# Kernel optimization log

Hardware: AMD Instinct MI355X
Metric: run time of the kernel (lower is better)

The kernel has to match this reference:

```python
import jax, jax.numpy as jnp
import numpy as np

PAD_token, SOS_token, EOS_token = 0, 1, 2
V, E, H, B, To, Ti = 10000, 512, 512, 32, 256, 1024


def _u(key, shape, fan_in):
    s = 1.0 / np.sqrt(fan_in)
    return jax.random.uniform(key, shape, jnp.float32, -s, s)


def setup_inputs() -> dict:
    key = jax.random.key(0)
    ks = jax.random.split(key, 16)
    inp = {
        "padded_input": jax.random.randint(ks[0], (B, To), 3, V),
        "encoder_padded_outputs": jax.random.normal(ks[1], (B, Ti, H), jnp.float32),
        "embedding": jax.random.normal(ks[2], (V, E), jnp.float32) * 0.02,
        # layer 0 LSTMCell: input = embed + encoder context (E + H)
        "Wih0": _u(ks[3], (4 * H, E + H), H), "Whh0": _u(ks[4], (4 * H, H), H),
        "bih0": _u(ks[5], (4 * H,), H),       "bhh0": _u(ks[6], (4 * H,), H),
        # layer 1 LSTMCell: input = H
        "Wih1": _u(ks[7], (4 * H, H), H),     "Whh1": _u(ks[8], (4 * H, H), H),
        "bih1": _u(ks[9], (4 * H,), H),       "bhh1": _u(ks[10], (4 * H,), H),
        # MLP: Linear(2H -> H), Tanh, Linear(H -> V)
        "W1": _u(ks[11], (H, 2 * H), 2 * H),  "b1": _u(ks[12], (H,), 2 * H),
        "W2": _u(ks[13], (V, H), H),          "b2": _u(ks[14], (V,), H),
    }
    return inp


def _lstm_cell(x, h, c, Wih, Whh, bih, bhh):
    g = x @ Wih.T + bih + h @ Whh.T + bhh            # [B, 4H]
    i, f, gg, o = jnp.split(g, 4, axis=-1)           # torch gate order i,f,g,o
    c2 = jax.nn.sigmoid(f) * c + jax.nn.sigmoid(i) * jnp.tanh(gg)
    h2 = jax.nn.sigmoid(o) * jnp.tanh(c2)
    return h2, c2


def reference(padded_input, encoder_padded_outputs, embedding,
              Wih0, Whh0, bih0, bhh0, Wih1, Whh1, bih1, bhh1,
              W1, b1, W2, b2):
    n = padded_input.shape[0]
    sos = jnp.full((n, 1), SOS_token, padded_input.dtype)
    eos = jnp.full((n, 1), EOS_token, padded_input.dtype)
    ys_in = jnp.concatenate([sos, padded_input], axis=1)   # [B, To+1]
    ys_out = jnp.concatenate([padded_input, eos], axis=1)  # [B, To+1]

    emb = embedding[ys_in]                                 # [B, To+1, E]
    emb_t = jnp.swapaxes(emb, 0, 1)                        # [To+1, B, E]
    enc = encoder_padded_outputs                           # [B, Ti, H]

    h0 = jnp.zeros((n, H), enc.dtype)
    init = (h0, h0, h0, h0, jnp.zeros((n, enc.shape[2]), enc.dtype))

    def step(carry, e_t):
        h_0, c_0, h_1, c_1, att_c = carry
        rnn_in = jnp.concatenate([e_t, att_c], axis=1)
        h_0, c_0 = _lstm_cell(rnn_in, h_0, c_0, Wih0, Whh0, bih0, bhh0)
        h_1, c_1 = _lstm_cell(h_0, h_1, c_1, Wih1, Whh1, bih1, bhh1)
        scores = jnp.einsum('bh,bth->bt', h_1, enc)        # [B, Ti]
        att_w = jax.nn.softmax(scores, axis=-1)
        att_c = jnp.einsum('bt,bth->bh', att_w, enc)       # [B, H]
        mlp_in = jnp.concatenate([h_1, att_c], axis=1)
        logits = jnp.tanh(mlp_in @ W1.T + b1) @ W2.T + b2  # [B, V]
        return (h_0, c_0, h_1, c_1, att_c), logits

    _, y_all = jax.lax.scan(step, init, emb_t)             # [To+1, B, V]
    logits = jnp.swapaxes(y_all, 0, 1).reshape(-1, V)      # [B*(To+1), V]
    labels = ys_out.reshape(-1)
    logp = jax.nn.log_softmax(logits, axis=-1)
    nll = -jnp.take_along_axis(logp, labels[:, None], axis=1)[:, 0]
    mask = (labels != PAD_token).astype(logits.dtype)
    loss = jnp.sum(nll * mask) / jnp.maximum(jnp.sum(mask), 1.0)
    return loss
```

## Files before the change

kernel.cpp:

```cpp
#include <hip/hip_runtime.h>
#include <hip/hip_bf16.h>

#define B_    32
#define TO_   256
#define T_    257
#define H_    512
#define V_    10000
#define TI_   1024
#define NROW_ 8224
#define NB_   256

using f32x4 = __attribute__((ext_vector_type(4))) float;
using s16x8 = __attribute__((ext_vector_type(8))) short;
typedef unsigned long long ull;

struct Ptrs {
  const int* padded;
  const float* enc;
  const float* emb;
  const float *Wih0, *Whh0, *bih0, *bhh0;
  const float *Wih1, *Whh1, *bih1, *bhh1;
  const float *W1, *b1, *W2, *b2;
  float* out;
  unsigned short *mlpin;
  unsigned short *embt;
  unsigned short *tanhv;
  unsigned short *W0c;
  unsigned short *W1c;
  unsigned short *W1b;
  unsigned short *W2b;
  float *bias0c, *bias1c;
  unsigned short *attc;
  float *upart;
  float *zp;
  unsigned short *Xh0;
  unsigned short *Xh1;
  float *Xh1f;
  unsigned *arrX;
  unsigned *arrY;
  unsigned *marr;
  unsigned *larr;
  unsigned *ibar;
  float *rowsum;
  float *lablog;
};

__device__ __forceinline__ unsigned short f2b(float f){
  __hip_bfloat16 h = __float2bfloat16(f);
  unsigned short r; __builtin_memcpy(&r, &h, 2); return r;
}
__device__ __forceinline__ float b2f(unsigned short u){
  unsigned v = ((unsigned)u) << 16; float f; __builtin_memcpy(&f, &v, 4); return f;
}
__device__ __forceinline__ float sigf(float x){ return 1.f / (1.f + expf(-x)); }

__device__ __forceinline__ float aldf(const float* p){
  return __hip_atomic_load(p, __ATOMIC_RELAXED, __HIP_MEMORY_SCOPE_AGENT);
}
__device__ __forceinline__ unsigned aldw(const unsigned* p){
  return __hip_atomic_load(p, __ATOMIC_RELAXED, __HIP_MEMORY_SCOPE_AGENT);
}
__device__ __forceinline__ ull aldu(const ull* p){
  return __hip_atomic_load(p, __ATOMIC_RELAXED, __HIP_MEMORY_SCOPE_AGENT);
}
__device__ __forceinline__ void astf(float* p, float v){
  __hip_atomic_store(p, v, __ATOMIC_RELAXED, __HIP_MEMORY_SCOPE_AGENT);
}
__device__ __forceinline__ void astu(ull* p, ull v){
  __hip_atomic_store(p, v, __ATOMIC_RELAXED, __HIP_MEMORY_SCOPE_AGENT);
}
__device__ __forceinline__ void astw(unsigned* p, unsigned v){
  __hip_atomic_store(p, v, __ATOMIC_RELAXED, __HIP_MEMORY_SCOPE_AGENT);
}
#define DRAIN asm volatile("s_waitcnt vmcnt(0)" ::: "memory")

__device__ __forceinline__ void gbarInit(unsigned* bar){
  DRAIN; __syncthreads();
  if (threadIdx.x < 64){
    const int l = threadIdx.x;
    if (l == 0) astw(bar + blockIdx.x * 4, 1u);
    for (;;){
      unsigned f0 = aldw(bar + (l      ) * 4);
      unsigned f1 = aldw(bar + (l +  64) * 4);
      unsigned f2 = aldw(bar + (l + 128) * 4);
      unsigned f3 = aldw(bar + (l + 192) * 4);
      if (__all((f0 >= 1u) & (f1 >= 1u) & (f2 >= 1u) & (f3 >= 1u))) break;
      __builtin_amdgcn_s_sleep(1);
    }
  }
  __syncthreads();
}

__global__ __launch_bounds__(256) void kprep(Ptrs P){
  const int stride = gridDim.x * blockDim.x;
  const int i0 = blockIdx.x * blockDim.x + threadIdx.x;
  for (int i = i0; i < 128 * 4; i += stride){ P.arrX[i] = 0u; P.arrY[i] = 0u; }
  for (int i = i0; i < 256 * 4; i += stride){ P.marr[i] = 0u; P.ibar[i] = 0u; }
  for (int i = i0; i < 32 * 4; i += stride) P.larr[i] = 0u;
  for (int i = i0; i < T_ * B_ * 512; i += stride){
    int k = i & 511, tb = i >> 9, b = tb & 31, t = tb >> 5;
    int tok = (t == 0) ? 1 : P.padded[b * TO_ + (t - 1)];
    P.embt[i] = f2b(P.emb[(size_t)tok * 512 + k]);
  }
  for (int i = i0; i < 2048 * 1536; i += stride){
    int k = i % 1536, gp = i / 1536;
    int j = gp >> 2, q = gp & 3, g = q * 512 + j;
    float v = (k < 1024) ? P.Wih0[(size_t)g * 1024 + k] : P.Whh0[(size_t)g * 512 + (k - 1024)];
    P.W0c[i] = f2b(v);
  }
  for (int i = i0; i < 2048 * 1024; i += stride){
    int k = i & 1023, gp = i >> 10;
    int j = gp >> 2, q = gp & 3, g = q * 512 + j;
    float v = (k < 512) ? P.Wih1[(size_t)g * 512 + k] : P.Whh1[(size_t)g * 512 + (k - 512)];
    P.W1c[i] = f2b(v);
  }
  for (int i = i0; i < 2048; i += stride){
    int j = i >> 2, q = i & 3, g = q * 512 + j;
    P.bias0c[i] = P.bih0[g] + P.bhh0[g];
    P.bias1c[i] = P.bih1[g] + P.bhh1[g];
  }
  for (int i = i0; i < 512 * 1024; i += stride) P.W1b[i] = f2b(P.W1[i]);
  for (int i = i0; i < NROW_; i += stride) P.rowsum[i] = 0.f;
}

__global__ __launch_bounds__(256) void kprep2(Ptrs P){
  const int stride = gridDim.x * blockDim.x;
  const int i0 = blockIdx.x * blockDim.x + threadIdx.x;
  for (int i = i0; i < V_ * 512; i += stride) P.W2b[i] = f2b(P.W2[i]);
}

__global__ __launch_bounds__(256, 1) void kA(Ptrs P){
  __shared__ __align__(16) unsigned short enc_s[128 * 512];
  __shared__ float h1_s[512];
  __shared__ float w_s[128];
  __shared__ float gate_s[2][32][17];
  __shared__ float h_s[32][4];
  __shared__ float zred[2];
  const int bb = blockIdx.x, tid = threadIdx.x;
  const int b_att = bb >> 3, tc = bb & 7;

  {
    const float* ep = P.enc + ((size_t)b_att * TI_ + (size_t)tc * 128) * H_;
    for (int idx = tid; idx < 128 * 512; idx += 256){
      int r = idx >> 9;
      unsigned byteoff = ((unsigned)idx * 2u) ^ ((unsigned)(r & 7) << 4);
      enc_s[byteoff >> 1] = f2b(ep[idx]);
    }
  }
  {
    int g = bb * 256 + tid;
    if (g < 16384){ astw((unsigned*)P.Xh0 + g, 0u); astw((unsigned*)P.Xh1 + g, 0u); }
    if (g < 32768) astf(P.Xh1f + g, 0.f);
    if (g < 8192)  astw((unsigned*)P.attc + g, 0u);
  }
  gbarInit(P.ibar);

  const int wv = tid >> 6, l = tid & 63, lr = l & 15, lk = l >> 4;
  const int bh = wv & 1, kh = wv >> 1;
  const int batch = bh * 16 + lr;
  const int eidx = tid - 128, eb = eidx >> 2, ejl = eidx & 3;
  const bool isGemm = bb < 128;
  const int rb = bb - 128; const bool isRed = (rb >= 0 && rb < 32);
  float c0r = 0.f, c1r = 0.f;

  for (int t = 0; t < T_; ++t){
    const int p = t & 1, pp = p ^ 1;
    const unsigned tv = (unsigned)t + 1u;
    if (isGemm){
      if (t > 0 && tid < 64){
        const unsigned want = tv - 1u;
        for (;;){
          unsigned f = (tid < 32) ? aldw(P.larr + tid * 4) : want;
          if (__all(f >= want)) break;
          __builtin_amdgcn_s_sleep(1);
        }
      }
      __syncthreads();
      {
        const unsigned short* Brow = P.W0c + (size_t)(bb * 16 + lr) * 1536;
        const unsigned short* Erow = P.embt + ((size_t)t * 32 + batch) * 512;
        const ull* Arow = (const ull*)(P.attc + batch * 512);
        const ull* Hrow = (const ull*)(P.Xh0 + pp * 16384 + batch * 512);
        f32x4 acc = {0.f, 0.f, 0.f, 0.f};
        #pragma unroll
        for (int ks = 0; ks < 8; ++ks){
          const int kb = (kh * 8 + ks) * 32 + lk * 8;
          s16x8 a = *(const s16x8*)(Erow + kb);
          s16x8 b = *(const s16x8*)(Brow + kb);
          acc = __builtin_amdgcn_mfma_f32_16x16x32_bf16(a, b, acc, 0, 0, 0);
        }
        #pragma unroll
        for (int ks = 0; ks < 8; ++ks){
          const int kb = (kh * 8 + ks) * 32 + lk * 8;
          ull d0 = aldu(Arow + (kb >> 2)), d1 = aldu(Arow + (kb >> 2) + 1);
          s16x8 a; __builtin_memcpy(&a, &d0, 8); __builtin_memcpy(((char*)&a) + 8, &d1, 8);
          s16x8 b = *(const s16x8*)(Brow + 512 + kb);
          acc = __builtin_amdgcn_mfma_f32_16x16x32_bf16(a, b, acc, 0, 0, 0);
        }
        #pragma unroll
        for (int ks = 0; ks < 8; ++ks){
          const int kb = (kh * 8 + ks) * 32 + lk * 8;
          ull d0 = aldu(Hrow + (kb >> 2)), d1 = aldu(Hrow + (kb >> 2) + 1);
          s16x8 a; __builtin_memcpy(&a, &d0, 8); __builtin_memcpy(((char*)&a) + 8, &d1, 8);
          s16x8 b = *(const s16x8*)(Brow + 1024 + kb);
          acc = __builtin_amdgcn_mfma_f32_16x16x32_bf16(a, b, acc, 0, 0, 0);
        }
        #pragma unroll
        for (int j = 0; j < 4; ++j) gate_s[kh][bh * 16 + lk * 4 + j][lr] = acc[j];
      }
      __syncthreads();
      if (tid >= 128){
        const float* bs = P.bias0c + bb * 16 + ejl * 4;
        float ii = sigf (gate_s[0][eb][ejl * 4 + 0] + gate_s[1][eb][ejl * 4 + 0] + bs[0]);
        float ff = sigf (gate_s[0][eb][ejl * 4 + 1] + gate_s[1][eb][ejl * 4 + 1] + bs[1]);
        float gg = tanhf(gate_s[0][eb][ejl * 4 + 2] + gate_s[1][eb][ejl * 4 + 2] + bs[2]);
        float oo = sigf (gate_s[0][eb][ejl * 4 + 3] + gate_s[1][eb][ejl * 4 + 3] + bs[3]);
        float cn = ff * c0r + ii * gg; c0r = cn;
        h_s[eb][ejl] = oo * tanhf(cn);
      }
      __syncthreads();
      if (tid < 32){
        unsigned short hb[4];
        #pragma unroll
        for (int jl = 0; jl < 4; ++jl) hb[jl] = f2b(h_s[tid][jl]);
        ull v; __builtin_memcpy(&v, hb, 8);
        astu((ull*)(P.Xh0 + p * 16384 + tid * 512 + bb * 4), v);
      }
      DRAIN; __syncthreads();
      if (tid < 64){
        if (tid == 0) astw(P.arrX + bb * 4, tv);
        for (;;){
          unsigned f0 = aldw(P.arrX + tid * 4), f1 = aldw(P.arrX + (tid + 64) * 4);
          if (__all((f0 >= tv) & (f1 >= tv))) break;
          __builtin_amdgcn_s_sleep(1);
        }
      }
      __syncthreads();
      {
        const unsigned short* Brow = P.W1c + (size_t)(bb * 16 + lr) * 1024;
        const ull* H0r = (const ull*)(P.Xh0 + p * 16384 + batch * 512);
        const ull* H1r = (const ull*)(P.Xh1 + pp * 16384 + batch * 512);
        f32x4 acc = {0.f, 0.f, 0.f, 0.f};
        #pragma unroll
        for (int ks = 0; ks < 8; ++ks){
          const int kb = (kh * 8 + ks) * 32 + lk * 8;
          ull d0 = aldu(H0r + (kb >> 2)), d1 = aldu(H0r + (kb >> 2) + 1);
          s16x8 a; __builtin_memcpy(&a, &d0, 8); __builtin_memcpy(((char*)&a) + 8, &d1, 8);
          s16x8 b = *(const s16x8*)(Brow + kb);
          acc = __builtin_amdgcn_mfma_f32_16x16x32_bf16(a, b, acc, 0, 0, 0);
        }
        #pragma unroll
        for (int ks = 0; ks < 8; ++ks){
          const int kb = (kh * 8 + ks) * 32 + lk * 8;
          ull d0 = aldu(H1r + (kb >> 2)), d1 = aldu(H1r + (kb >> 2) + 1);
          s16x8 a; __builtin_memcpy(&a, &d0, 8); __builtin_memcpy(((char*)&a) + 8, &d1, 8);
          s16x8 b = *(const s16x8*)(Brow + 512 + kb);
          acc = __builtin_amdgcn_mfma_f32_16x16x32_bf16(a, b, acc, 0, 0, 0);
        }
        #pragma unroll
        for (int j = 0; j < 4; ++j) gate_s[kh][bh * 16 + lk * 4 + j][lr] = acc[j];
      }
      __syncthreads();
      if (tid >= 128){
        const float* bs = P.bias1c + bb * 16 + ejl * 4;
        float ii = sigf (gate_s[0][eb][ejl * 4 + 0] + gate_s[1][eb][ejl * 4 + 0] + bs[0]);
        float ff = sigf (gate_s[0][eb][ejl * 4 + 1] + gate_s[1][eb][ejl * 4 + 1] + bs[1]);
        float gg = tanhf(gate_s[0][eb][ejl * 4 + 2] + gate_s[1][eb][ejl * 4 + 2] + bs[2]);
        float oo = sigf (gate_s[0][eb][ejl * 4 + 3] + gate_s[1][eb][ejl * 4 + 3] + bs[3]);
        float cn = ff * c1r + ii * gg; c1r = cn;
        h_s[eb][ejl] = oo * tanhf(cn);
      }
      __syncthreads();
      if (tid < 32){
        unsigned short hb[4];
        #pragma unroll
        for (int jl = 0; jl < 4; ++jl) hb[jl] = f2b(h_s[tid][jl]);
        ull vb; __builtin_memcpy(&vb, hb, 8);
        astu((ull*)(P.Xh1 + p * 16384 + tid * 512 + bb * 4), vb);
        *(ull*)(P.mlpin + ((size_t)t * 32 + tid) * 1024 + bb * 4) = vb;
        ull w0, w1;
        __builtin_memcpy(&w0, &h_s[tid][0], 8);
        __builtin_memcpy(&w1, &h_s[tid][2], 8);
        ull* dst = (ull*)P.Xh1f + ((p * 16384 + tid * 512 + bb * 4) >> 1);
        astu(dst, w0); astu(dst + 1, w1);
      }
      DRAIN; __syncthreads();
      if (tid == 0) astw(P.arrY + bb * 4, tv);
    }
    if (tid < 64){
      for (;;){
        unsigned f0 = aldw(P.arrY + tid * 4), f1 = aldw(P.arrY + (tid + 64) * 4);
        if (__all((f0 >= tv) & (f1 >= tv))) break;
        __builtin_amdgcn_s_sleep(1);
      }
    }
    __syncthreads();
    {
      ull v = aldu((const ull*)(P.Xh1f + p * 16384 + b_att * 512) + tid);
      float f2[2]; __builtin_memcpy(f2, &v, 8);
      h1_s[tid * 2] = f2[0]; h1_s[tid * 2 + 1] = f2[1];
    }
    __syncthreads();
    {
      const int ti_l = tid >> 1, half = tid & 1;
      float s = 0.f;
      const unsigned swz = (unsigned)(ti_l & 7) << 4;
      for (int h8 = half * 256; h8 < half * 256 + 256; h8 += 8){
        unsigned byteoff = ((unsigned)(ti_l * 512 + h8) * 2u) ^ swz;
        s16x8 ev = *(const s16x8*)((const char*)enc_s + byteoff);
        #pragma unroll
        for (int e = 0; e < 8; ++e) s += b2f((unsigned short)ev[e]) * h1_s[h8 + e];
      }
      s += __shfl_xor(s, 1);
      if (half == 0) w_s[ti_l] = expf(s);
    }
    __syncthreads();
    {
      if (tid < 128){
        float z = w_s[tid];
        #pragma unroll
        for (int off = 1; off < 64; off <<= 1) z += __shfl_xor(z, off);
        if ((tid & 63) == 0) zred[tid >> 6] = z;
      }
      float a0 = 0.f, a1 = 0.f;
      const int hc = tid * 2;
      for (int ti = 0; ti < 128; ++ti){
        const float wvv = w_s[ti];
        unsigned byteoff = ((unsigned)(ti * 1024 + hc * 2)) ^ ((unsigned)(ti & 7) << 4);
        unsigned pk = *(const unsigned*)((const char*)enc_s + byteoff);
        a0 += wvv * b2f((unsigned short)(pk & 0xffffu));
        a1 += wvv * b2f((unsigned short)(pk >> 16));
      }
      float f2[2] = {a0, a1};
      ull pv; __builtin_memcpy(&pv, f2, 8);
      astu((ull*)(P.upart + ((size_t)b_att * 8 + tc) * 512 + hc), pv);
      __syncthreads();
      if (tid == 0) astf(P.zp + b_att * 8 + tc, zred[0] + zred[1]);
      DRAIN; __syncthreads();
      if (tid == 0) astw(P.marr + (b_att * 8 + tc) * 4, tv);
    }
    if (isRed){
      if (tid < 64){
        for (;;){
          unsigned f = (tid < 8) ? aldw(P.marr + (rb * 8 + tid) * 4) : tv;
          if (__all(f >= tv)) break;
          __builtin_amdgcn_s_sleep(1);
        }
      }
      __syncthreads();
      const int hc = tid * 2;
      float s0 = 0.f, s1 = 0.f, zs = 0.f;
      #pragma unroll
      for (int c = 0; c < 8; ++c){
        ull v = aldu((const ull*)(P.upart + ((size_t)rb * 8 + c) * 512 + hc));
        float f2[2]; __builtin_memcpy(f2, &v, 8);
        s0 += f2[0]; s1 += f2[1];
        zs += aldf(P.zp + rb * 8 + c);
      }
      const float rZ = 1.f / zs;
      unsigned pk = (unsigned)f2b(s0 * rZ) | ((unsigned)f2b(s1 * rZ) << 16);
      astw(((unsigned*)P.attc) + rb * 256 + tid, pk);
      *(unsigned*)(P.mlpin + ((size_t)t * 32 + rb) * 1024 + 512 + hc) = pk;
      DRAIN; __syncthreads();
      if (tid == 0) astw(P.larr + rb * 4, tv);
    }
  }
}

__global__ __launch_bounds__(256) void kB1(Ptrs P){
  const int wid = blockIdx.x * 4 + (threadIdx.x >> 6);
  if (wid >= 129 * 8) return;
  const int mt = wid >> 3, nt = wid & 7;
  const int l = threadIdx.x & 63, lr = l & 15, lk = l >> 4;
  const int mr = mt * 64, nc = nt * 64;
  f32x4 acc[4][4] = {};
  for (int k0 = 0; k0 < 1024; k0 += 32){
    s16x8 af[4], bfm[4];
    #pragma unroll
    for (int f = 0; f < 4; ++f){
      int row = mr + f * 16 + lr; if (row > NROW_ - 1) row = NROW_ - 1;
      af[f] = *(const s16x8*)(P.mlpin + (size_t)row * 1024 + k0 + lk * 8);
      int col = nc + f * 16 + lr;
      bfm[f] = *(const s16x8*)(P.W1b + (size_t)col * 1024 + k0 + lk * 8);
    }
    #pragma unroll
    for (int fi = 0; fi < 4; ++fi)
      #pragma unroll
      for (int fj = 0; fj < 4; ++fj)
        acc[fi][fj] = __builtin_amdgcn_mfma_f32_16x16x32_bf16(af[fi], bfm[fj], acc[fi][fj], 0, 0, 0);
  }
  #pragma unroll
  for (int fi = 0; fi < 4; ++fi){
    #pragma unroll
    for (int jj = 0; jj < 4; ++jj){
      int m = mr + fi * 16 + lk * 4 + jj;
      if (m >= NROW_) continue;
      #pragma unroll
      for (int fj = 0; fj < 4; ++fj){
        int n = nc + fj * 16 + lr;
        P.tanhv[(size_t)m * 512 + n] = f2b(tanhf(acc[fi][fj][jj] + P.b1[n]));
      }
    }
  }
}

__global__ __launch_bounds__(256) void kB2(Ptrs P){
  const int wid = blockIdx.x * 4 + (threadIdx.x >> 6);
  if (wid >= 129 * 157) return;
  const int mt = wid / 157, nt = wid % 157;
  const int l = threadIdx.x & 63, lr = l & 15, lk = l >> 4;
  const int mr = mt * 64, nc = nt * 64;
  f32x4 acc[4][4] = {};
  for (int k0 = 0; k0 < 512; k0 += 32){
    s16x8 af[4], bfm[4];
    #pragma unroll
    for (int f = 0; f < 4; ++f){
      int row = mr + f * 16 + lr; if (row > NROW_ - 1) row = NROW_ - 1;
      af[f] = *(const s16x8*)(P.tanhv + (size_t)row * 512 + k0 + lk * 8);
      int col = nc + f * 16 + lr; if (col > V_ - 1) col = V_ - 1;
      bfm[f] = *(const s16x8*)(P.W2b + (size_t)col * 512 + k0 + lk * 8);
    }
    #pragma unroll
    for (int fi = 0; fi < 4; ++fi)
      #pragma unroll
      for (int fj = 0; fj < 4; ++fj)
        acc[fi][fj] = __builtin_amdgcn_mfma_f32_16x16x32_bf16(af[fi], bfm[fj], acc[fi][fj], 0, 0, 0);
  }
  #pragma unroll
  for (int fi = 0; fi < 4; ++fi){
    #pragma unroll
    for (int jj = 0; jj < 4; ++jj){
      const int m = mr + fi * 16 + lk * 4 + jj;
      float s = 0.f;
      #pragma unroll
      for (int fj = 0; fj < 4; ++fj){
        int n = nc + fj * 16 + lr;
        if (n < V_) s += expf(acc[fi][fj][jj] + P.b2[n]);
      }
      s += __shfl_xor(s, 1); s += __shfl_xor(s, 2);
      s += __shfl_xor(s, 4); s += __shfl_xor(s, 8);
      if (lr == 0 && m < NROW_) unsafeAtomicAdd(P.rowsum + m, s);
    }
  }
}

__global__ __launch_bounds__(256) void kL1(Ptrs P){
  const int wid = blockIdx.x * 4 + (threadIdx.x >> 6);
  if (wid >= NROW_) return;
  const int l = threadIdx.x & 63;
  const int t = wid >> 5, b = wid & 31;
  const int lab = (t < TO_) ? P.padded[b * TO_ + t] : 2;
  float s = 0.f;
  s16x8 av = *(const s16x8*)(P.tanhv + (size_t)wid * 512 + l * 8);
  s16x8 wv = *(const s16x8*)(P.W2b + (size_t)lab * 512 + l * 8);
  #pragma unroll
  for (int e = 0; e < 8; ++e) s += b2f((unsigned short)av[e]) * b2f((unsigned short)wv[e]);
  #pragma unroll
  for (int off = 1; off < 64; off <<= 1) s += __shfl_xor(s, off);
  if (l == 0) P.lablog[wid] = s + P.b2[lab];
}

__global__ __launch_bounds__(512) void kL2(Ptrs P){
  __shared__ float ssum[8], scnt[8];
  const int tid = threadIdx.x;
  float sum = 0.f, cnt = 0.f;
  for (int r = tid; r < NROW_; r += 512){
    int t = r >> 5, b = r & 31;
    int lab = (t < TO_) ? P.padded[b * TO_ + t] : 2;
    if (lab != 0){ sum += logf(P.rowsum[r]) - P.lablog[r]; cnt += 1.f; }
  }
  #pragma unroll
  for (int off = 1; off < 64; off <<= 1){ sum += __shfl_xor(sum, off); cnt += __shfl_xor(cnt, off); }
  if ((tid & 63) == 0){ ssum[tid >> 6] = sum; scnt[tid >> 6] = cnt; }
  __syncthreads();
  if (tid == 0){
    float S = 0.f, C = 0.f;
    for (int i = 0; i < 8; ++i){ S += ssum[i]; C += scnt[i]; }
    P.out[0] = S / fmaxf(C, 1.f);
  }
}

extern "C" void kernel_launch(void* const* d_in, const int* in_sizes, int n_in,
                              void* d_out, int out_size, void* d_ws, size_t ws_size,
                              hipStream_t stream){
  (void)in_sizes; (void)n_in; (void)out_size; (void)ws_size;
  Ptrs P;
  P.padded = (const int*)d_in[0];
  P.enc    = (const float*)d_in[1];
  P.emb    = (const float*)d_in[2];
  P.Wih0 = (const float*)d_in[3];  P.Whh0 = (const float*)d_in[4];
  P.bih0 = (const float*)d_in[5];  P.bhh0 = (const float*)d_in[6];
  P.Wih1 = (const float*)d_in[7];  P.Whh1 = (const float*)d_in[8];
  P.bih1 = (const float*)d_in[9];  P.bhh1 = (const float*)d_in[10];
  P.W1 = (const float*)d_in[11];   P.b1 = (const float*)d_in[12];
  P.W2 = (const float*)d_in[13];   P.b2 = (const float*)d_in[14];
  P.out = (float*)d_out;

  char* w = (char*)d_ws;
  size_t off = 0;
  auto take = [&](size_t bytes) -> void* {
    void* ptr = (void*)(w + off);
    off += (bytes + 255) & ~(size_t)255;
    return ptr;
  };
  P.mlpin  = (unsigned short*)take((size_t)T_ * B_ * 1024 * 2);
  P.embt   = (unsigned short*)take((size_t)T_ * B_ * 512 * 2);
  P.tanhv  = P.embt;
  P.W0c    = (unsigned short*)take((size_t)2048 * 1536 * 2);
  P.W1c    = (unsigned short*)take((size_t)2048 * 1024 * 2);
  P.W2b    = P.W0c;
  P.W1b    = (unsigned short*)take((size_t)512 * 1024 * 2);
  P.bias0c = (float*)take(2048 * 4);
  P.bias1c = (float*)take(2048 * 4);
  P.attc   = (unsigned short*)take(32 * 512 * 2);
  P.upart  = (float*)take((size_t)32 * 8 * 512 * 4);
  P.zp     = (float*)take(32 * 8 * 4);
  P.Xh0    = (unsigned short*)take(2 * 32 * 512 * 2);
  P.Xh1    = (unsigned short*)take(2 * 32 * 512 * 2);
  P.Xh1f   = (float*)take(2 * 32 * 512 * 4);
  P.arrX   = (unsigned*)take(128 * 4 * 4);
  P.arrY   = (unsigned*)take(128 * 4 * 4);
  P.marr   = (unsigned*)take(256 * 4 * 4);
  P.larr   = (unsigned*)take(32 * 4 * 4);
  P.ibar   = (unsigned*)take(256 * 4 * 4);
  P.rowsum = (float*)take(NROW_ * 4);
  P.lablog = (float*)take(NROW_ * 4);

  kprep<<<dim3(2048), dim3(256), 0, stream>>>(P);
  void* args[] = { (void*)&P };
  hipLaunchCooperativeKernel(kA, dim3(NB_), dim3(256), args, 0, stream);
  kprep2<<<dim3(1024), dim3(256), 0, stream>>>(P);
  kB1<<<dim3(258),  dim3(256), 0, stream>>>(P);
  kB2<<<dim3(5064), dim3(256), 0, stream>>>(P);
  kL1<<<dim3(2056), dim3(256), 0, stream>>>(P);
  kL2<<<dim3(1),    dim3(512), 0, stream>>>(P);
}
```

Before: 7.714 ms.

## Replace flag barriers with step-tagged data words in persistent LSTM kernel

Each shared value (h0, h1, h1 float, attention partials, Z partials, attention context) is now stored as a 64-bit word whose high half holds the step tag. Consumers spin on the data itself instead of waiting on separate arrival flags behind drains and block barriers. Independent work is reordered ahead of the waits: the embedding and recurrent-h GEMM parts run before polling for the attention context or h0. This removes the DRAIN/syncthreads/flag round trips per phase, but doubles the traffic for these buffers, and the spin caps can silently let stale data through.

After: 8.726 ms. 1.13x slower.

```diff
diff --git a/kernel.cpp b/kernel.cpp
--- a/kernel.cpp
+++ b/kernel.cpp
@@ -9,6 +9,7 @@
 #define TI_   1024
 #define NROW_ 8224
 #define NB_   256
+#define SPINCAP 150000
 
 using f32x4 = __attribute__((ext_vector_type(4))) float;
 using s16x8 = __attribute__((ext_vector_type(8))) short;
@@ -30,17 +31,12 @@
   unsigned short *W1b;
   unsigned short *W2b;
   float *bias0c, *bias1c;
-  unsigned short *attc;
-  float *upart;
-  float *zp;
-  unsigned short *Xh0;
-  unsigned short *Xh1;
-  float *Xh1f;
-  unsigned *arrX;
-  unsigned *arrY;
-  unsigned *marr;
-  unsigned *larr;
-  unsigned *ibar;
+  ull *h0T;
+  ull *h1T;
+  ull *h1fT;
+  ull *upT;
+  ull *zpT;
+  ull *atT;
   float *rowsum;
   float *lablog;
 };
@@ -54,49 +50,23 @@
 }
 __device__ __forceinline__ float sigf(float x){ return 1.f / (1.f + expf(-x)); }
 
-__device__ __forceinline__ float aldf(const float* p){
-  return __hip_atomic_load(p, __ATOMIC_RELAXED, __HIP_MEMORY_SCOPE_AGENT);
-}
-__device__ __forceinline__ unsigned aldw(const unsigned* p){
-  return __hip_atomic_load(p, __ATOMIC_RELAXED, __HIP_MEMORY_SCOPE_AGENT);
-}
 __device__ __forceinline__ ull aldu(const ull* p){
   return __hip_atomic_load(p, __ATOMIC_RELAXED, __HIP_MEMORY_SCOPE_AGENT);
 }
-__device__ __forceinline__ void astf(float* p, float v){
-  __hip_atomic_store(p, v, __ATOMIC_RELAXED, __HIP_MEMORY_SCOPE_AGENT);
-}
 __device__ __forceinline__ void astu(ull* p, ull v){
   __hip_atomic_store(p, v, __ATOMIC_RELAXED, __HIP_MEMORY_SCOPE_AGENT);
 }
-__device__ __forceinline__ void astw(unsigned* p, unsigned v){
-  __hip_atomic_store(p, v, __ATOMIC_RELAXED, __HIP_MEMORY_SCOPE_AGENT);
-}
 #define DRAIN asm volatile("s_waitcnt vmcnt(0)" ::: "memory")
-
-__device__ __forceinline__ void gbarInit(unsigned* bar){
-  DRAIN; __syncthreads();
-  if (threadIdx.x < 64){
-    const int l = threadIdx.x;
-    if (l == 0) astw(bar + blockIdx.x * 4, 1u);
-    for (;;){
-      unsigned f0 = aldw(bar + (l      ) * 4);
-      unsigned f1 = aldw(bar + (l +  64) * 4);
-      unsigned f2 = aldw(bar + (l + 128) * 4);
-      unsigned f3 = aldw(bar + (l + 192) * 4);
-      if (__all((f0 >= 1u) & (f1 >= 1u) & (f2 >= 1u) & (f3 >= 1u))) break;
-      __builtin_amdgcn_s_sleep(1);
-    }
-  }
-  __syncthreads();
-}
+#define TAG(v) ((unsigned)((v) >> 32))
+#define LO(v)  ((unsigned)(v))
 
 __global__ __launch_bounds__(256) void kprep(Ptrs P){
   const int stride = gridDim.x * blockDim.x;
   const int i0 = blockIdx.x * blockDim.x + threadIdx.x;
-  for (int i = i0; i < 128 * 4; i += stride){ P.arrX[i] = 0u; P.arrY[i] = 0u; }
-  for (int i = i0; i < 256 * 4; i += stride){ P.marr[i] = 0u; P.ibar[i] = 0u; }
-  for (int i = i0; i < 32 * 4; i += stride) P.larr[i] = 0u;
+  for (int i = i0; i < 2 * 32 * 256; i += stride){ P.h0T[i] = 0; P.h1T[i] = 0; P.atT[i] = 0; }
+  for (int i = i0; i < 2 * 32 * 512; i += stride) P.h1fT[i] = 0;
+  for (int i = i0; i < 2 * 32 * 8 * 512; i += stride) P.upT[i] = 0;
+  for (int i = i0; i < 2 * 32 * 8; i += stride) P.zpT[i] = 0;
   for (int i = i0; i < T_ * B_ * 512; i += stride){
     int k = i & 511, tb = i >> 9, b = tb & 31, t = tb >> 5;
     int tok = (t == 0) ? 1 : P.padded[b * TO_ + (t - 1)];
@@ -142,72 +112,78 @@
   {
     const float* ep = P.enc + ((size_t)b_att * TI_ + (size_t)tc * 128) * H_;
     for (int idx = tid; idx < 128 * 512; idx += 256){
-      int r = idx >> 9;
-      unsigned byteoff = ((unsigned)idx * 2u) ^ ((unsigned)(r & 7) << 4);
+      int row = idx >> 9;
+      unsigned byteoff = ((unsigned)idx * 2u) ^ ((unsigned)(row & 7) << 4);
       enc_s[byteoff >> 1] = f2b(ep[idx]);
     }
   }
-  {
-    int g = bb * 256 + tid;
-    if (g < 16384){ astw((unsigned*)P.Xh0 + g, 0u); astw((unsigned*)P.Xh1 + g, 0u); }
-    if (g < 32768) astf(P.Xh1f + g, 0.f);
-    if (g < 8192)  astw((unsigned*)P.attc + g, 0u);
-  }
-  gbarInit(P.ibar);
 
   const int wv = tid >> 6, l = tid & 63, lr = l & 15, lk = l >> 4;
   const int bh = wv & 1, kh = wv >> 1;
   const int batch = bh * 16 + lr;
   const int eidx = tid - 128, eb = eidx >> 2, ejl = eidx & 3;
   const bool isGemm = bb < 128;
-  const int rb = bb - 128; const bool isRed = (rb >= 0 && rb < 32);
+  const bool isRed = (bb >= 128 && bb < 160);
+  const int rb = bb - 128;
   float c0r = 0.f, c1r = 0.f;
 
   for (int t = 0; t < T_; ++t){
     const int p = t & 1, pp = p ^ 1;
     const unsigned tv = (unsigned)t + 1u;
     if (isGemm){
-      if (t > 0 && tid < 64){
-        const unsigned want = tv - 1u;
+      const unsigned short* Brow = P.W0c + (size_t)(bb * 16 + lr) * 1536;
+      const unsigned short* Erow = P.embt + ((size_t)t * 32 + batch) * 512;
+      f32x4 acc = {0.f, 0.f, 0.f, 0.f};
+      #pragma unroll
+      for (int ks = 0; ks < 8; ++ks){
+        const int kb = (kh * 8 + ks) * 32 + lk * 8;
+        s16x8 a = *(const s16x8*)(Erow + kb);
+        s16x8 b = *(const s16x8*)(Brow + kb);
+        acc = __builtin_amdgcn_mfma_f32_16x16x32_bf16(a, b, acc, 0, 0, 0);
+      }
+      {
+        const ull* H = P.h0T + (size_t)(pp * 32 + batch) * 256;
+        #pragma unroll
+        for (int ks = 0; ks < 8; ++ks){
+          const int u = (kh * 8 + ks) * 16 + lk * 4;
+          ull d0 = aldu(H + u), d1 = aldu(H + u + 1), d2 = aldu(H + u + 2), d3 = aldu(H + u + 3);
+          s16x8 a; unsigned* ap = (unsigned*)&a;
+          ap[0] = LO(d0); ap[1] = LO(d1); ap[2] = LO(d2); ap[3] = LO(d3);
+          s16x8 b = *(const s16x8*)(Brow + 1024 + (kh * 8 + ks) * 32 + lk * 8);
+          acc = __builtin_amdgcn_mfma_f32_16x16x32_bf16(a, b, acc, 0, 0, 0);
+        }
+      }
+      ull av[32];
+      {
+        const ull* A = P.atT + (size_t)(pp * 32 + batch) * 256;
+        const unsigned want = (unsigned)t;
+        int spin = 0;
         for (;;){
-          unsigned f = (tid < 32) ? aldw(P.larr + tid * 4) : want;
-          if (__all(f >= want)) break;
+          bool ok = true;
+          #pragma unroll
+          for (int ks = 0; ks < 8; ++ks){
+            const int u = (kh * 8 + ks) * 16 + lk * 4;
+            #pragma unroll
+            for (int q = 0; q < 4; ++q){
+              av[ks * 4 + q] = aldu(A + u + q);
+              ok &= (TAG(av[ks * 4 + q]) >= want);
+            }
+          }
+          if (__all(ok)) break;
+          if (++spin > SPINCAP) break;
           __builtin_amdgcn_s_sleep(1);
         }
       }
-      __syncthreads();
-      {
-        const unsigned short* Brow = P.W0c + (size_t)(bb * 16 + lr) * 1536;
-        const unsigned short* Erow = P.embt + ((size_t)t * 32 + batch) * 512;
-        const ull* Arow = (const ull*)(P.attc + batch * 512);
-        const ull* Hrow = (const ull*)(P.Xh0 + pp * 16384 + batch * 512);
-        f32x4 acc = {0.f, 0.f, 0.f, 0.f};
-        #pragma unroll
-        for (int ks = 0; ks < 8; ++ks){
-          const int kb = (kh * 8 + ks) * 32 + lk * 8;
-          s16x8 a = *(const s16x8*)(Erow + kb);
-          s16x8 b = *(const s16x8*)(Brow + kb);
-          acc = __builtin_amdgcn_mfma_f32_16x16x32_bf16(a, b, acc, 0, 0, 0);
-        }
-        #pragma unroll
-        for (int ks = 0; ks < 8; ++ks){
-          const int kb = (kh * 8 + ks) * 32 + lk * 8;
-          ull d0 = aldu(Arow + (kb >> 2)), d1 = aldu(Arow + (kb >> 2) + 1);
-          s16x8 a; __builtin_memcpy(&a, &d0, 8); __builtin_memcpy(((char*)&a) + 8, &d1, 8);
-          s16x8 b = *(const s16x8*)(Brow + 512 + kb);
-          acc = __builtin_amdgcn_mfma_f32_16x16x32_bf16(a, b, acc, 0, 0, 0);
-        }
-        #pragma unroll
-        for (int ks = 0; ks < 8; ++ks){
-          const int kb = (kh * 8 + ks) * 32 + lk * 8;
-          ull d0 = aldu(Hrow + (kb >> 2)), d1 = aldu(Hrow + (kb >> 2) + 1);
-          s16x8 a; __builtin_memcpy(&a, &d0, 8); __builtin_memcpy(((char*)&a) + 8, &d1, 8);
-          s16x8 b = *(const s16x8*)(Brow + 1024 + kb);
-          acc = __builtin_amdgcn_mfma_f32_16x16x32_bf16(a, b, acc, 0, 0, 0);
-        }
-        #pragma unroll
-        for (int j = 0; j < 4; ++j) gate_s[kh][bh * 16 + lk * 4 + j][lr] = acc[j];
-      }
+      #pragma unroll
+      for (int ks = 0; ks < 8; ++ks){
+        s16x8 a; unsigned* ap = (unsigned*)&a;
+        ap[0] = LO(av[ks * 4 + 0]); ap[1] = LO(av[ks * 4 + 1]);
+        ap[2] = LO(av[ks * 4 + 2]); ap[3] = LO(av[ks * 4 + 3]);
+        s16x8 b = *(const s16x8*)(Brow + 512 + (kh * 8 + ks) * 32 + lk * 8);
+        acc = __builtin_amdgcn_mfma_f32_16x16x32_bf16(a, b, acc, 0, 0, 0);
+      }
+      #pragma unroll
+      for (int j = 0; j < 4; ++j) gate_s[kh][bh * 16 + lk * 4 + j][lr] = acc[j];
       __syncthreads();
       if (tid >= 128){
         const float* bs = P.bias0c + bb * 16 + ejl * 4;
@@ -220,46 +196,55 @@
       }
       __syncthreads();
       if (tid < 32){
-        unsigned short hb[4];
+        unsigned lo0 = (unsigned)f2b(h_s[tid][0]) | ((unsigned)f2b(h_s[tid][1]) << 16);
+        unsigned lo1 = (unsigned)f2b(h_s[tid][2]) | ((unsigned)f2b(h_s[tid][3]) << 16);
+        ull* D = P.h0T + (size_t)(p * 32 + tid) * 256 + bb * 2;
+        astu(D,     (ull)lo0 | ((ull)tv << 32));
+        astu(D + 1, (ull)lo1 | ((ull)tv << 32));
+      }
+      const unsigned short* Brow1 = P.W1c + (size_t)(bb * 16 + lr) * 1024;
+      f32x4 acc2 = {0.f, 0.f, 0.f, 0.f};
+      {
+        const ull* H = P.h1T + (size_t)(pp * 32 + batch) * 256;
         #pragma unroll
-        for (int jl = 0; jl < 4; ++jl) hb[jl] = f2b(h_s[tid][jl]);
-        ull v; __builtin_memcpy(&v, hb, 8);
-        astu((ull*)(P.Xh0 + p * 16384 + tid * 512 + bb * 4), v);
-      }
-      DRAIN; __syncthreads();
-      if (tid < 64){
-        if (tid == 0) astw(P.arrX + bb * 4, tv);
+        for (int ks = 0; ks < 8; ++ks){
+          const int u = (kh * 8 + ks) * 16 + lk * 4;
+          ull d0 = aldu(H + u), d1 = aldu(H + u + 1), d2 = aldu(H + u + 2), d3 = aldu(H + u + 3);
+          s16x8 a; unsigned* ap = (unsigned*)&a;
+          ap[0] = LO(d0); ap[1] = LO(d1); ap[2] = LO(d2); ap[3] = LO(d3);
+          s16x8 b = *(const s16x8*)(Brow1 + 512 + (kh * 8 + ks) * 32 + lk * 8);
+          acc2 = __builtin_amdgcn_mfma_f32_16x16x32_bf16(a, b, acc2, 0, 0, 0);
+        }
+      }
+      {
+        const ull* H = P.h0T + (size_t)(p * 32 + batch) * 256;
+        int spin = 0;
         for (;;){
-          unsigned f0 = aldw(P.arrX + tid * 4), f1 = aldw(P.arrX + (tid + 64) * 4);
-          if (__all((f0 >= tv) & (f1 >= tv))) break;
+          bool ok = true;
+          #pragma unroll
+          for (int ks = 0; ks < 8; ++ks){
+            const int u = (kh * 8 + ks) * 16 + lk * 4;
+            #pragma unroll
+            for (int q = 0; q < 4; ++q){
+              av[ks * 4 + q] = aldu(H + u + q);
+              ok &= (TAG(av[ks * 4 + q]) >= tv);
+            }
+          }
+          if (__all(ok)) break;
+          if (++spin > SPINCAP) break;
           __builtin_amdgcn_s_sleep(1);
         }
       }
-      __syncthreads();
-      {
-        const unsigned short* Brow = P.W1c + (size_t)(bb * 16 + lr) * 1024;
-        const ull* H0r = (const ull*)(P.Xh0 + p * 16384 + batch * 512);
-        const ull* H1r = (const ull*)(P.Xh1 + pp * 16384 + batch * 512);
-        f32x4 acc = {0.f, 0.f, 0.f, 0.f};
-        #pragma unroll
-        for (int ks = 0; ks < 8; ++ks){
-          const int kb = (kh * 8 + ks) * 32 + lk * 8;
-          ull d0 = aldu(H0r + (kb >> 2)), d1 = aldu(H0r + (kb >> 2) + 1);
-          s16x8 a; __builtin_memcpy(&a, &d0, 8); __builtin_memcpy(((char*)&a) + 8, &d1, 8);
-          s16x8 b = *(const s16x8*)(Brow + kb);
-          acc = __builtin_amdgcn_mfma_f32_16x16x32_bf16(a, b, acc, 0, 0, 0);
-        }
-        #pragma unroll
-        for (int ks = 0; ks < 8; ++ks){
-          const int kb = (kh * 8 + ks) * 32 + lk * 8;
-          ull d0 = aldu(H1r + (kb >> 2)), d1 = aldu(H1r + (kb >> 2) + 1);
-          s16x8 a; __builtin_memcpy(&a, &d0, 8); __builtin_memcpy(((char*)&a) + 8, &d1, 8);
-          s16x8 b = *(const s16x8*)(Brow + 512 + kb);
-          acc = __builtin_amdgcn_mfma_f32_16x16x32_bf16(a, b, acc, 0, 0, 0);
-        }
-        #pragma unroll
-        for (int j = 0; j < 4; ++j) gate_s[kh][bh * 16 + lk * 4 + j][lr] = acc[j];
-      }
+      #pragma unroll
+      for (int ks = 0; ks < 8; ++ks){
+        s16x8 a; unsigned* ap = (unsigned*)&a;
+        ap[0] = LO(av[ks * 4 + 0]); ap[1] = LO(av[ks * 4 + 1]);
+        ap[2] = LO(av[ks * 4 + 2]); ap[3] = LO(av[ks * 4 + 3]);
+        s16x8 b = *(const s16x8*)(Brow1 + (kh * 8 + ks) * 32 + lk * 8);
+        acc2 = __builtin_amdgcn_mfma_f32_16x16x32_bf16(a, b, acc2, 0, 0, 0);
+      }
+      #pragma unroll
+      for (int j = 0; j < 4; ++j) gate_s[kh][bh * 16 + lk * 4 + j][lr] = acc2[j];
       __syncthreads();
       if (tid >= 128){
         const float* bs = P.bias1c + bb * 16 + ejl * 4;
@@ -272,33 +257,33 @@
       }
       __syncthreads();
       if (tid < 32){
-        unsigned short hb[4];
+        unsigned lo0 = (unsigned)f2b(h_s[tid][0]) | ((unsigned)f2b(h_s[tid][1]) << 16);
+        unsigned lo1 = (unsigned)f2b(h_s[tid][2]) | ((unsigned)f2b(h_s[tid][3]) << 16);
+        ull* D = P.h1T + (size_t)(p * 32 + tid) * 256 + bb * 2;
+        astu(D,     (ull)lo0 | ((ull)tv << 32));
+        astu(D + 1, (ull)lo1 | ((ull)tv << 32));
+        ull hv = (ull)lo0 | ((ull)lo1 << 32);
+        *(ull*)(P.mlpin + ((size_t)t * 32 + tid) * 1024 + bb * 4) = hv;
+        DRAIN;
+        ull* F = P.h1fT + (size_t)(p * 32 + tid) * 512 + bb * 4;
         #pragma unroll
-        for (int jl = 0; jl < 4; ++jl) hb[jl] = f2b(h_s[tid][jl]);
-        ull vb; __builtin_memcpy(&vb, hb, 8);
-        astu((ull*)(P.Xh1 + p * 16384 + tid * 512 + bb * 4), vb);
-        *(ull*)(P.mlpin + ((size_t)t * 32 + tid) * 1024 + bb * 4) = vb;
-        ull w0, w1;
-        __builtin_memcpy(&w0, &h_s[tid][0], 8);
-        __builtin_memcpy(&w1, &h_s[tid][2], 8);
-        ull* dst = (ull*)P.Xh1f + ((p * 16384 + tid * 512 + bb * 4) >> 1);
-        astu(dst, w0); astu(dst + 1, w1);
-      }
-      DRAIN; __syncthreads();
-      if (tid == 0) astw(P.arrY + bb * 4, tv);
-    }
-    if (tid < 64){
+        for (int jl = 0; jl < 4; ++jl)
+          astu(F + jl, (ull)__float_as_uint(h_s[tid][jl]) | ((ull)tv << 32));
+      }
+    }
+    {
+      const ull* Hf = P.h1fT + (size_t)(p * 32 + b_att) * 512 + tid * 2;
+      ull v0 = 0, v1 = 0;
+      int spin = 0;
       for (;;){
-        unsigned f0 = aldw(P.arrY + tid * 4), f1 = aldw(P.arrY + (tid + 64) * 4);
-        if (__all((f0 >= tv) & (f1 >= tv))) break;
+        v0 = aldu(Hf); v1 = aldu(Hf + 1);
+        bool ok = (TAG(v0) >= tv) & (TAG(v1) >= tv);
+        if (__all(ok)) break;
+        if (++spin > SPINCAP) break;
         __builtin_amdgcn_s_sleep(1);
       }
-    }
-    __syncthreads();
-    {
-      ull v = aldu((const ull*)(P.Xh1f + p * 16384 + b_att * 512) + tid);
-      float f2[2]; __builtin_memcpy(f2, &v, 8);
-      h1_s[tid * 2] = f2[0]; h1_s[tid * 2 + 1] = f2[1];
+      h1_s[tid * 2]     = __uint_as_float(LO(v0));
+      h1_s[tid * 2 + 1] = __uint_as_float(LO(v1));
     }
     __syncthreads();
     {
@@ -331,38 +316,43 @@
         a0 += wvv * b2f((unsigned short)(pk & 0xffffu));
         a1 += wvv * b2f((unsigned short)(pk >> 16));
       }
-      float f2[2] = {a0, a1};
-      ull pv; __builtin_memcpy(&pv, f2, 8);
-      astu((ull*)(P.upart + ((size_t)b_att * 8 + tc) * 512 + hc), pv);
+      ull* U = P.upT + ((size_t)(p * 32 + b_att) * 8 + tc) * 512 + hc;
+      astu(U,     (ull)__float_as_uint(a0) | ((ull)tv << 32));
+      astu(U + 1, (ull)__float_as_uint(a1) | ((ull)tv << 32));
       __syncthreads();
-      if (tid == 0) astf(P.zp + b_att * 8 + tc, zred[0] + zred[1]);
-      DRAIN; __syncthreads();
-      if (tid == 0) astw(P.marr + (b_att * 8 + tc) * 4, tv);
+      if (tid == 0)
+        astu(P.zpT + (size_t)(p * 32 + b_att) * 8 + tc,
+             (ull)__float_as_uint(zred[0] + zred[1]) | ((ull)tv << 32));
     }
     if (isRed){
-      if (tid < 64){
-        for (;;){
-          unsigned f = (tid < 8) ? aldw(P.marr + (rb * 8 + tid) * 4) : tv;
-          if (__all(f >= tv)) break;
-          __builtin_amdgcn_s_sleep(1);
+      const ull* ub = P.upT + ((size_t)(p * 32 + rb) * 8) * 512 + tid * 2;
+      const ull* zb = P.zpT + (size_t)(p * 32 + rb) * 8;
+      ull u0[8], u1[8], zv[8];
+      int spin = 0;
+      for (;;){
+        bool ok = true;
+        #pragma unroll
+        for (int c = 0; c < 8; ++c){
+          u0[c] = aldu(ub + c * 512);
+          u1[c] = aldu(ub + c * 512 + 1);
+          zv[c] = aldu(zb + c);
+          ok &= (TAG(u0[c]) >= tv) & (TAG(u1[c]) >= tv) & (TAG(zv[c]) >= tv);
         }
-      }
-      __syncthreads();
-      const int hc = tid * 2;
+        if (__all(ok)) break;
+        if (++spin > SPINCAP) break;
+        __builtin_amdgcn_s_sleep(1);
+      }
       float s0 = 0.f, s1 = 0.f, zs = 0.f;
       #pragma unroll
       for (int c = 0; c < 8; ++c){
-        ull v = aldu((const ull*)(P.upart + ((size_t)rb * 8 + c) * 512 + hc));
-        float f2[2]; __builtin_memcpy(f2, &v, 8);
-        s0 += f2[0]; s1 += f2[1];
-        zs += aldf(P.zp + rb * 8 + c);
+        s0 += __uint_as_float(LO(u0[c]));
+        s1 += __uint_as_float(LO(u1[c]));
+        zs += __uint_as_float(LO(zv[c]));
       }
       const float rZ = 1.f / zs;
       unsigned pk = (unsigned)f2b(s0 * rZ) | ((unsigned)f2b(s1 * rZ) << 16);
-      astw(((unsigned*)P.attc) + rb * 256 + tid, pk);
-      *(unsigned*)(P.mlpin + ((size_t)t * 32 + rb) * 1024 + 512 + hc) = pk;
-      DRAIN; __syncthreads();
-      if (tid == 0) astw(P.larr + rb * 4, tv);
+      astu(P.atT + (size_t)(p * 32 + rb) * 256 + tid, (ull)pk | ((ull)tv << 32));
+      *(unsigned*)(P.mlpin + ((size_t)t * 32 + rb) * 1024 + 512 + tid * 2) = pk;
     }
   }
 }
@@ -464,10 +454,10 @@
   __shared__ float ssum[8], scnt[8];
   const int tid = threadIdx.x;
   float sum = 0.f, cnt = 0.f;
-  for (int r = tid; r < NROW_; r += 512){
-    int t = r >> 5, b = r & 31;
+  for (int rr = tid; rr < NROW_; rr += 512){
+    int t = rr >> 5, b = rr & 31;
     int lab = (t < TO_) ? P.padded[b * TO_ + t] : 2;
-    if (lab != 0){ sum += logf(P.rowsum[r]) - P.lablog[r]; cnt += 1.f; }
+    if (lab != 0){ sum += logf(P.rowsum[rr]) - P.lablog[rr]; cnt += 1.f; }
   }
   #pragma unroll
   for (int off = 1; off < 64; off <<= 1){ sum += __shfl_xor(sum, off); cnt += __shfl_xor(cnt, off); }
@@ -512,17 +502,12 @@
   P.W1b    = (unsigned short*)take((size_t)512 * 1024 * 2);
   P.bias0c = (float*)take(2048 * 4);
   P.bias1c = (float*)take(2048 * 4);
-  P.attc   = (unsigned short*)take(32 * 512 * 2);
-  P.upart  = (float*)take((size_t)32 * 8 * 512 * 4);
-  P.zp     = (float*)take(32 * 8 * 4);
-  P.Xh0    = (unsigned short*)take(2 * 32 * 512 * 2);
-  P.Xh1    = (unsigned short*)take(2 * 32 * 512 * 2);
-  P.Xh1f   = (float*)take(2 * 32 * 512 * 4);
-  P.arrX   = (unsigned*)take(128 * 4 * 4);
-  P.arrY   = (unsigned*)take(128 * 4 * 4);
-  P.marr   = (unsigned*)take(256 * 4 * 4);
-  P.larr   = (unsigned*)take(32 * 4 * 4);
-  P.ibar   = (unsigned*)take(256 * 4 * 4);
+  P.h0T    = (ull*)take((size_t)2 * 32 * 256 * 8);
+  P.h1T    = (ull*)take((size_t)2 * 32 * 256 * 8);
+  P.h1fT   = (ull*)take((size_t)2 * 32 * 512 * 8);
+  P.upT    = (ull*)take((size_t)2 * 32 * 8 * 512 * 8);
+  P.zpT    = (ull*)take((size_t)2 * 32 * 8 * 8);
+  P.atT    = (ull*)take((size_t)2 * 32 * 256 * 8);
   P.rowsum = (float*)take(NROW_ * 4);
   P.lablog = (float*)take(NROW_ * 4);
 
```
